# Performance work log

Measured on AMD Instinct MI355X. Metric: run time of the kernel, lower is better.

Reference implementation:

```python
import jax, jax.numpy as jnp
import numpy as np

T, B, C, H, L = 256, 128, 512, 512, 2
WSCALE = 0.03  # keep gates out of hard saturation


def setup_inputs() -> dict:
    key = jax.random.key(0)
    k1, k2, k3 = jax.random.split(key, 3)
    return {
        "input_tensor": jax.random.normal(k1, (T, B, C), jnp.float32),  # (t, b, c), batch_first=False
        "h0": jnp.zeros((L, 4, B, H), jnp.float32),  # per layer: h, c, h_inner, c_inner
        "Wg": jax.random.normal(k2, (L, 4 * H, C + H), jnp.float32) * WSCALE,  # outer Gates
        "bg": jnp.zeros((L, 4 * H), jnp.float32),
        "Wi": jax.random.normal(k3, (L, 4 * H, 2 * H), jnp.float32) * WSCALE,  # inner LSTMCell Gates
        "bi": jnp.zeros((L, 4 * H), jnp.float32),
    }


def _nested_lstm_layer(x, state, Wg, bg, Wi, bi):
    # x: [T, B, C]; state: (h, c, h_inner, c_inner) each [B, H]
    def step(carry, x_t):
        h, c, hi, ci = carry
        # outer cell gates
        g = jnp.concatenate([x_t, h], axis=1) @ Wg.T + bg  # [B, 4H]
        i, f, o, gc = jnp.split(g, 4, axis=1)
        cell = jax.nn.sigmoid(f) * c + jax.nn.sigmoid(i) * jnp.tanh(gc)
        # inner LSTMCell, input = outer candidate cell
        g2 = jnp.concatenate([cell, hi], axis=1) @ Wi.T + bi  # [B, 4H]
        i2, f2, o2, g2c = jnp.split(g2, 4, axis=1)
        ci_n = jax.nn.sigmoid(f2) * ci + jax.nn.sigmoid(i2) * jnp.tanh(g2c)
        hi_n = jax.nn.sigmoid(o2) * jnp.tanh(ci_n)
        # outer cell state is replaced by inner hidden; outer hidden gated on it
        h_n = jax.nn.sigmoid(o) * jnp.tanh(hi_n)
        return (h_n, hi_n, hi_n, ci_n), h_n

    carry, ys = jax.lax.scan(step, state, x)
    return ys, carry  # ys: [T, B, H]


def reference(input_tensor, h0, Wg, bg, Wi, bi):
    x = input_tensor  # already (t, b, c); scan over leading time axis
    n_layers = Wg.shape[0]
    for l in range(n_layers):
        state = (h0[l, 0], h0[l, 1], h0[l, 2], h0[l, 3])
        x, _ = _nested_lstm_layer(x, state, Wg[l], bg[l], Wi[l], bi[l])
    # return_all_layers=False -> last layer output, shape (t, b, h)
    return x
```

## Files before the change

### kernel.cpp

```cpp
#include <hip/hip_runtime.h>

#define T_DIM 256
#define B_DIM 128
#define C_DIM 512
#define H_DIM 512

#define R0H 0
#define R1H 16384
#define R2H 32768
#define PLB 98304

typedef _Float16 half8 __attribute__((ext_vector_type(8)));
typedef float f32x4 __attribute__((ext_vector_type(4)));
typedef unsigned u32x4 __attribute__((ext_vector_type(4)));

__device__ __forceinline__ float sigf(float x) { return 1.0f / (1.0f + __expf(-x)); }
__device__ __forceinline__ float tanhf_(float x) {
  float e = __expf(2.0f * x);
  return (e - 1.0f) / (e + 1.0f);
}

__device__ __forceinline__ half8 cvt8(float4 a, float4 b) {
  half8 h;
  h[0] = (_Float16)a.x; h[1] = (_Float16)a.y; h[2] = (_Float16)a.z; h[3] = (_Float16)a.w;
  h[4] = (_Float16)b.x; h[5] = (_Float16)b.y; h[6] = (_Float16)b.z; h[7] = (_Float16)b.w;
  return h;
}

__device__ __forceinline__ void gbar_arrive(unsigned* slots, int bc, unsigned epoch) {
  __syncthreads();
  if (threadIdx.x == 0) *(volatile unsigned*)(slots + bc) = epoch;
}

__device__ __forceinline__ void gbar_wait_pw(const unsigned* slots, unsigned epoch,
                                             int pollwave) {
  if ((int)(threadIdx.x >> 6) == pollwave) {
    const volatile unsigned* myslot =
        (const volatile unsigned*)(slots + (threadIdx.x & 31));
    int guard = 0;
    for (;;) {
      asm volatile("buffer_inv sc0\n\ts_waitcnt vmcnt(0)" ::: "memory");
      unsigned v = *myslot;
      if (__ballot(v >= epoch) == ~0ull) break;
      if (++guard > (1 << 14)) break;
    }
  }
  __syncthreads();
  asm volatile("buffer_inv sc0" ::: "memory");
  asm volatile("s_waitcnt vmcnt(0)" ::: "memory");
}

__device__ __forceinline__ unsigned sysld_u32(const unsigned* p) {
  unsigned v;
  asm volatile("global_load_dword %0, %1, off sc0 sc1\n\ts_waitcnt vmcnt(0)"
               : "=v"(v) : "v"(p) : "memory");
  return v;
}

__device__ __forceinline__ void xpoll_raw(const unsigned* slots, unsigned epoch) {
  const unsigned* my = slots + (threadIdx.x & 31);
  int guard = 0;
  for (;;) {
    unsigned v = sysld_u32(my);
    if (__ballot(v >= epoch) == ~0ull) break;
    if (++guard > (1 << 15)) break;
  }
}

__device__ __forceinline__ void xpost(unsigned* flag, unsigned epoch) {
  asm volatile("s_waitcnt vmcnt(0)" ::: "memory");
  asm volatile("global_store_dword %0, %1, off sc0 sc1" ::
                   "v"(flag), "v"(epoch) : "memory");
}

__device__ __forceinline__ void store_llc_h16(_Float16* p, _Float16 v) {
  unsigned u = (unsigned)__builtin_bit_cast(unsigned short, v);
  asm volatile("global_store_short %0, %1, off sc0 sc1" ::
                   "v"(p), "v"(u) : "memory");
}

__global__ __launch_bounds__(256, 1) void nlstm_pipe(
    const float* __restrict__ xin, const float* __restrict__ h0,
    const float* __restrict__ Wg, const float* __restrict__ bgb,
    const float* __restrict__ Wi, const float* __restrict__ bib,
    float* __restrict__ out, unsigned* __restrict__ bar,
    _Float16* __restrict__ y0buf, _Float16* __restrict__ hlcb,
    _Float16* __restrict__ hicb, _Float16* __restrict__ clcb)
{
  __shared__ __align__(16) char smem[131072];
  _Float16* AldsH = (_Float16*)smem;
  float* Pl = (float*)(smem + PLB);

  const int tid  = threadIdx.x;
  const int xcd  = blockIdx.x & 7;
  const int lyr  = xcd >> 2;
  const int pgrp = xcd & 3;
  const int bc   = blockIdx.x >> 3;
  const int wv   = tid >> 6;
  const int lane = tid & 63;
  const int ln   = lane & 15;
  const int kg   = lane >> 4;
  const int pb   = tid >> 4;
  const int pj   = tid & 15;
  const int jglob = bc * 16 + pj;
  const int ncol  = bc * 16 + ln;
  const int r0    = pgrp * 32;

  const int exo = (jglob >> 5) * 1024 + (((jglob >> 3) & 3) * 16 + pb) * 8 + (jglob & 7);

  unsigned* eslots = bar + xcd * 64;
  unsigned* cslots = eslots + 32;
  unsigned* fwdS = bar + 512 + pgrp * 32;
  unsigned* bakS = bar + 640 + pgrp * 32;

  _Float16* hloc0 = hlcb + ((size_t)xcd * 2 + 0) * 16384;
  _Float16* hloc1 = hlcb + ((size_t)xcd * 2 + 1) * 16384;
  _Float16* hilc0 = hicb + ((size_t)xcd * 2 + 0) * 16384;
  _Float16* hilc1 = hicb + ((size_t)xcd * 2 + 1) * 16384;
  _Float16* cbase = clcb + (size_t)xcd * 16384;
  _Float16* y0base = y0buf + (size_t)pgrp * 4 * 16384;

  half8 wgf[4][8], wif[4][8];
  float bgv[4], biv[4];
#pragma unroll
  for (int g = 0; g < 4; ++g) {
    const float* wgr = Wg + ((size_t)lyr * 2048 + g * 512 + ncol) * 1024 + wv * 256;
    const float* wir = Wi + ((size_t)lyr * 2048 + g * 512 + ncol) * 1024 + wv * 256;
#pragma unroll
    for (int i = 0; i < 8; ++i) {
      const float* p = wgr + i * 32 + kg * 8;
      wgf[g][i] = cvt8(*(const float4*)p, *(const float4*)(p + 4));
      const float* q = wir + i * 32 + kg * 8;
      wif[g][i] = cvt8(*(const float4*)q, *(const float4*)(q + 4));
    }
    bgv[g] = bgb[lyr * 2048 + g * 512 + jglob];
    biv[g] = bib[lyr * 2048 + g * 512 + jglob];
  }

  float st_c[2], st_ci[2], o_pre[2];
  {
    const float* h0l = h0 + (size_t)lyr * 4 * B_DIM * H_DIM + (size_t)(r0 + pb) * H_DIM + jglob;
#pragma unroll
    for (int mt = 0; mt < 2; ++mt) {
      const float* pp = h0l + (size_t)mt * 16 * H_DIM;
      float h_in  = pp[0];
      st_c[mt]    = pp[(size_t)1 * B_DIM * H_DIM];
      float hi_in = pp[(size_t)2 * B_DIM * H_DIM];
      st_ci[mt]   = pp[(size_t)3 * B_DIM * H_DIM];
      hloc0[exo + mt * 512] = (_Float16)h_in;
      hilc0[exo + mt * 512] = (_Float16)hi_in;
      o_pre[mt] = 0.f;
    }
  }

  auto stage_x = [&](int t) {
    const int m = tid & 31;
    const int q = tid >> 5;
    const int mt = m >> 4, mm = m & 15;
    const float* srow = xin + ((size_t)t * B_DIM + r0 + m) * C_DIM;
#pragma unroll
    for (int i = 0; i < 8; ++i) {
      const int chunk = q * 8 + i;
      const int ks = chunk >> 2, kq = chunk & 3;
      const float* p = srow + chunk * 8;
      *(half8*)(AldsH + R0H + ks * 1024 + mt * 512 + (kq * 16 + mm) * 8) =
          cvt8(*(const float4*)p, *(const float4*)(p + 4));
    }
  };
  auto copy_hhi = [&](const _Float16* hrd, const _Float16* hird) {
    u32x4 vh[8], vy[8];
#pragma unroll
    for (int i = 0; i < 8; ++i) vh[i] = *(const u32x4*)(hrd + (i * 256 + tid) * 8);
#pragma unroll
    for (int i = 0; i < 8; ++i) vy[i] = *(const u32x4*)(hird + (i * 256 + tid) * 8);
#pragma unroll
    for (int i = 0; i < 8; ++i) *(u32x4*)(AldsH + R1H + (i * 256 + tid) * 8) = vh[i];
#pragma unroll
    for (int i = 0; i < 8; ++i) *(u32x4*)(AldsH + R2H + (i * 256 + tid) * 8) = vy[i];
  };
  auto copy_r0 = [&](const _Float16* src) {
    u32x4 v[8];
#pragma unroll
    for (int i = 0; i < 8; ++i) v[i] = *(const u32x4*)(src + (i * 256 + tid) * 8);
#pragma unroll
    for (int i = 0; i < 8; ++i) *(u32x4*)(AldsH + R0H + (i * 256 + tid) * 8) = v[i];
  };
  auto copy_r0_sys = [&](const _Float16* src) {
    u32x4 v[8];
#pragma unroll
    for (int i = 0; i < 8; ++i) {
      const u32x4* p = (const u32x4*)(src + (i * 256 + tid) * 8);
      asm volatile("global_load_dwordx4 %0, %1, off sc0 sc1"
                   : "=v"(v[i]) : "v"(p) : "memory");
    }
    asm volatile("s_waitcnt vmcnt(0)" ::: "memory");
    __builtin_amdgcn_sched_barrier(0);
#pragma unroll
    for (int i = 0; i < 8; ++i)
      *(u32x4*)(AldsH + R0H + (i * 256 + tid) * 8) = v[i];
  };
  auto mfma8 = [&](const _Float16* rb, int ksb, half8 (&wf)[4][8], f32x4 (&acc)[2][4]) {
#pragma unroll
    for (int i = 0; i < 8; ++i) {
      const _Float16* ab = rb + (ksb + i) * 1024 + lane * 8;
      half8 a0 = *(const half8*)(ab);
      half8 a1 = *(const half8*)(ab + 512);
#pragma unroll
      for (int g = 0; g < 4; ++g) {
        acc[0][g] = __builtin_amdgcn_mfma_f32_16x16x32_f16(a0, wf[g][i], acc[0][g], 0, 0, 0);
        acc[1][g] = __builtin_amdgcn_mfma_f32_16x16x32_f16(a1, wf[g][i], acc[1][g], 0, 0, 0);
      }
    }
  };
  auto plw = [&](f32x4 (&acc)[2][4]) {
#pragma unroll
    for (int mt = 0; mt < 2; ++mt)
#pragma unroll
      for (int g = 0; g < 4; ++g)
#pragma unroll
        for (int rr = 0; rr < 4; ++rr)
          Pl[(((g * 2 + mt) * 16 + kg * 4 + rr) * 16 + ln) * 4 + (wv ^ kg)] = acc[mt][g][rr];
  };
  auto plsum = [&](int g, int mt) -> float {
    f32x4 v = *(const f32x4*)(Pl + (((g * 2 + mt) * 16 + pb) * 16 + pj) * 4);
    return v[0] + v[1] + v[2] + v[3];
  };

  unsigned eseq = 0, cseq = 0;

  gbar_arrive(eslots, bc, ++eseq);
  if (lyr == 0) stage_x(0);
  gbar_wait_pw(eslots, eseq, 3);
  if (lyr == 1) {
    if (wv == 0) xpoll_raw(fwdS, 1u);
    __syncthreads();
    copy_r0_sys(y0base + 0);
    __syncthreads();
    if (tid == 0) xpost(bakS + bc, 1u);
  }
  if (wv < 2) {
    f32x4 acc[2][4];
#pragma unroll
    for (int mt = 0; mt < 2; ++mt)
#pragma unroll
      for (int g = 0; g < 4; ++g) acc[mt][g] = (f32x4){0.f, 0.f, 0.f, 0.f};
    mfma8(AldsH + R0H, 8 * wv, wgf, acc);
    plw(acc);
  }

  for (int t = 0; t < T_DIM; ++t) {
    const int pr = t & 1;
    _Float16* hrd  = pr ? hloc1 : hloc0;
    _Float16* hwr  = pr ? hloc0 : hloc1;
    _Float16* hird = pr ? hilc1 : hilc0;
    _Float16* hiwr = pr ? hilc0 : hilc1;
    _Float16* y0wr = y0base + (size_t)(t & 3) * 16384;
    _Float16* y0rd = y0base + (size_t)((t + 1) & 3) * 16384;

    copy_hhi(hrd, hird);
    __syncthreads();

    if (wv >= 2) {
      f32x4 acc[2][4];
#pragma unroll
      for (int mt = 0; mt < 2; ++mt)
#pragma unroll
        for (int g = 0; g < 4; ++g) acc[mt][g] = (f32x4){0.f, 0.f, 0.f, 0.f};
      mfma8(AldsH + R1H, 8 * wv - 16, wgf, acc);
      plw(acc);
    }
    __syncthreads();

#pragma unroll
    for (int mt = 0; mt < 2; ++mt) {
      float gi = plsum(0, mt) + bgv[0];
      float gf = plsum(1, mt) + bgv[1];
      float go = plsum(2, mt) + bgv[2];
      float gc = plsum(3, mt) + bgv[3];
      float cell = sigf(gf) * st_c[mt] + sigf(gi) * tanhf_(gc);
      o_pre[mt] = go;
      cbase[exo + mt * 512] = (_Float16)cell;
    }
    gbar_arrive(cslots, bc, ++cseq);
    if (wv >= 2) {
      f32x4 acc[2][4];
#pragma unroll
      for (int mt = 0; mt < 2; ++mt)
#pragma unroll
        for (int g = 0; g < 4; ++g) acc[mt][g] = (f32x4){0.f, 0.f, 0.f, 0.f};
      mfma8(AldsH + R2H, 8 * wv - 16, wif, acc);
      plw(acc);
    }
    gbar_wait_pw(cslots, cseq, 0);

    copy_r0(cbase);
    __syncthreads();

    if (wv < 2) {
      f32x4 acc[2][4];
#pragma unroll
      for (int mt = 0; mt < 2; ++mt)
#pragma unroll
        for (int g = 0; g < 4; ++g) acc[mt][g] = (f32x4){0.f, 0.f, 0.f, 0.f};
      mfma8(AldsH + R0H, 8 * wv, wif, acc);
      plw(acc);
    }
    __syncthreads();

#pragma unroll
    for (int mt = 0; mt < 2; ++mt) {
      float i2 = plsum(0, mt) + biv[0];
      float f2 = plsum(1, mt) + biv[1];
      float o2 = plsum(2, mt) + biv[2];
      float c2 = plsum(3, mt) + biv[3];
      float ci_n = sigf(f2) * st_ci[mt] + sigf(i2) * tanhf_(c2);
      float hi_n = sigf(o2) * tanhf_(ci_n);
      float h_n  = sigf(o_pre[mt]) * tanhf_(hi_n);
      st_ci[mt] = ci_n;
      st_c[mt]  = hi_n;
      hiwr[exo + mt * 512] = (_Float16)hi_n;
      hwr[exo + mt * 512]  = (_Float16)h_n;
      if (lyr == 0) {
        store_llc_h16(y0wr + exo + mt * 512, (_Float16)h_n);
      } else {
        out[((size_t)t * B_DIM + (r0 + pb + mt * 16)) * H_DIM + jglob] = h_n;
      }
    }

    gbar_arrive(eslots, bc, ++eseq);
    if (lyr == 0) {
      if (tid == 0) xpost(fwdS + bc, (unsigned)(t + 1));
      if (t + 1 < T_DIM) {
        stage_x(t + 1);
        __syncthreads();
        if (wv < 2) {
          f32x4 acc[2][4];
#pragma unroll
          for (int mt = 0; mt < 2; ++mt)
#pragma unroll
            for (int g = 0; g < 4; ++g) acc[mt][g] = (f32x4){0.f, 0.f, 0.f, 0.f};
          mfma8(AldsH + R0H, 8 * wv, wgf, acc);
          plw(acc);
        } else if (wv == 3 && t >= 2) {
          xpoll_raw(bakS, (unsigned)(t - 2));
        }
      }
    } else if (t + 1 < T_DIM) {
      if (wv == 0) xpoll_raw(fwdS, (unsigned)(t + 2));
      __syncthreads();
      copy_r0_sys(y0rd);
      __syncthreads();
      if (tid == 0) xpost(bakS + bc, (unsigned)(t + 2));
      if (wv < 2) {
        f32x4 acc[2][4];
#pragma unroll
        for (int mt = 0; mt < 2; ++mt)
#pragma unroll
          for (int g = 0; g < 4; ++g) acc[mt][g] = (f32x4){0.f, 0.f, 0.f, 0.f};
        mfma8(AldsH + R0H, 8 * wv, wgf, acc);
        plw(acc);
      }
    }
    gbar_wait_pw(eslots, eseq, 3);
  }
}

extern "C" void kernel_launch(void* const* d_in, const int* in_sizes, int n_in,
                              void* d_out, int out_size, void* d_ws, size_t ws_size,
                              hipStream_t stream) {
  const float* xin = (const float*)d_in[0];
  const float* h0  = (const float*)d_in[1];
  const float* Wg  = (const float*)d_in[2];
  const float* bg  = (const float*)d_in[3];
  const float* Wi  = (const float*)d_in[4];
  const float* bi  = (const float*)d_in[5];
  float* out = (float*)d_out;

  unsigned* bar  = (unsigned*)d_ws;
  _Float16* y0b  = (_Float16*)((char*)d_ws + 4096);
  _Float16* hlcb = y0b + (size_t)4 * 4 * 16384;
  _Float16* hicb = hlcb + (size_t)8 * 2 * 16384;
  _Float16* clcb = hicb + (size_t)8 * 2 * 16384;

  hipMemsetAsync(d_ws, 0, 4096, stream);

  nlstm_pipe<<<dim3(256), dim3(256), 0, stream>>>(
      xin, h0, Wg, bg, Wi, bi, out, bar, y0b, hlcb, hicb, clcb);
}
```

Baseline: 2.412 ms.

## Feed MFMA operands directly from global state buffers instead of LDS staging

The per-step copies of h, h_inner and the cell buffer into shared memory are removed, along with their block barriers. The MFMA routine now reads these operands straight from the global ping-pong buffers, and shared memory shrinks to 64KB. Layer-1 output stores are also deferred until after the barrier arrive, so they no longer sit on the critical path. The trade-off is that matrix operands now come from L2 with higher latency inside the inner MFMA loop rather than from LDS.

```diff
diff --git a/kernel.cpp b/kernel.cpp
--- a/kernel.cpp
+++ b/kernel.cpp
@@ -6,9 +6,7 @@
 #define H_DIM 512
 
 #define R0H 0
-#define R1H 16384
-#define R2H 32768
-#define PLB 98304
+#define PLB 32768
 
 typedef _Float16 half8 __attribute__((ext_vector_type(8)));
 typedef float f32x4 __attribute__((ext_vector_type(4)));
@@ -87,7 +85,7 @@
     _Float16* __restrict__ y0buf, _Float16* __restrict__ hlcb,
     _Float16* __restrict__ hicb, _Float16* __restrict__ clcb)
 {
-  __shared__ __align__(16) char smem[131072];
+  __shared__ __align__(16) char smem[65536];
   _Float16* AldsH = (_Float16*)smem;
   float* Pl = (float*)(smem + PLB);
 
@@ -137,7 +135,7 @@
     biv[g] = bib[lyr * 2048 + g * 512 + jglob];
   }
 
-  float st_c[2], st_ci[2], o_pre[2];
+  float st_c[2], st_ci[2], o_pre[2], outv[2];
   {
     const float* h0l = h0 + (size_t)lyr * 4 * B_DIM * H_DIM + (size_t)(r0 + pb) * H_DIM + jglob;
 #pragma unroll
@@ -150,6 +148,7 @@
       hloc0[exo + mt * 512] = (_Float16)h_in;
       hilc0[exo + mt * 512] = (_Float16)hi_in;
       o_pre[mt] = 0.f;
+      outv[mt] = 0.f;
     }
   }
 
@@ -166,24 +165,6 @@
       *(half8*)(AldsH + R0H + ks * 1024 + mt * 512 + (kq * 16 + mm) * 8) =
           cvt8(*(const float4*)p, *(const float4*)(p + 4));
     }
-  };
-  auto copy_hhi = [&](const _Float16* hrd, const _Float16* hird) {
-    u32x4 vh[8], vy[8];
-#pragma unroll
-    for (int i = 0; i < 8; ++i) vh[i] = *(const u32x4*)(hrd + (i * 256 + tid) * 8);
-#pragma unroll
-    for (int i = 0; i < 8; ++i) vy[i] = *(const u32x4*)(hird + (i * 256 + tid) * 8);
-#pragma unroll
-    for (int i = 0; i < 8; ++i) *(u32x4*)(AldsH + R1H + (i * 256 + tid) * 8) = vh[i];
-#pragma unroll
-    for (int i = 0; i < 8; ++i) *(u32x4*)(AldsH + R2H + (i * 256 + tid) * 8) = vy[i];
-  };
-  auto copy_r0 = [&](const _Float16* src) {
-    u32x4 v[8];
-#pragma unroll
-    for (int i = 0; i < 8; ++i) v[i] = *(const u32x4*)(src + (i * 256 + tid) * 8);
-#pragma unroll
-    for (int i = 0; i < 8; ++i) *(u32x4*)(AldsH + R0H + (i * 256 + tid) * 8) = v[i];
   };
   auto copy_r0_sys = [&](const _Float16* src) {
     u32x4 v[8];
@@ -257,16 +238,13 @@
     _Float16* y0wr = y0base + (size_t)(t & 3) * 16384;
     _Float16* y0rd = y0base + (size_t)((t + 1) & 3) * 16384;
 
-    copy_hhi(hrd, hird);
-    __syncthreads();
-
     if (wv >= 2) {
       f32x4 acc[2][4];
 #pragma unroll
       for (int mt = 0; mt < 2; ++mt)
 #pragma unroll
         for (int g = 0; g < 4; ++g) acc[mt][g] = (f32x4){0.f, 0.f, 0.f, 0.f};
-      mfma8(AldsH + R1H, 8 * wv - 16, wgf, acc);
+      mfma8(hrd, 8 * wv - 16, wgf, acc);
       plw(acc);
     }
     __syncthreads();
@@ -288,13 +266,10 @@
       for (int mt = 0; mt < 2; ++mt)
 #pragma unroll
         for (int g = 0; g < 4; ++g) acc[mt][g] = (f32x4){0.f, 0.f, 0.f, 0.f};
-      mfma8(AldsH + R2H, 8 * wv - 16, wif, acc);
+      mfma8(hird, 8 * wv - 16, wif, acc);
       plw(acc);
     }
     gbar_wait_pw(cslots, cseq, 0);
-
-    copy_r0(cbase);
-    __syncthreads();
 
     if (wv < 2) {
       f32x4 acc[2][4];
@@ -302,7 +277,7 @@
       for (int mt = 0; mt < 2; ++mt)
 #pragma unroll
         for (int g = 0; g < 4; ++g) acc[mt][g] = (f32x4){0.f, 0.f, 0.f, 0.f};
-      mfma8(AldsH + R0H, 8 * wv, wif, acc);
+      mfma8(cbase, 8 * wv, wif, acc);
       plw(acc);
     }
     __syncthreads();
@@ -323,7 +298,7 @@
       if (lyr == 0) {
         store_llc_h16(y0wr + exo + mt * 512, (_Float16)h_n);
       } else {
-        out[((size_t)t * B_DIM + (r0 + pb + mt * 16)) * H_DIM + jglob] = h_n;
+        outv[mt] = h_n;
       }
     }
 
@@ -345,20 +320,25 @@
           xpoll_raw(bakS, (unsigned)(t - 2));
         }
       }
-    } else if (t + 1 < T_DIM) {
-      if (wv == 0) xpoll_raw(fwdS, (unsigned)(t + 2));
-      __syncthreads();
-      copy_r0_sys(y0rd);
-      __syncthreads();
-      if (tid == 0) xpost(bakS + bc, (unsigned)(t + 2));
-      if (wv < 2) {
-        f32x4 acc[2][4];
-#pragma unroll
-        for (int mt = 0; mt < 2; ++mt)
-#pragma unroll
-          for (int g = 0; g < 4; ++g) acc[mt][g] = (f32x4){0.f, 0.f, 0.f, 0.f};
-        mfma8(AldsH + R0H, 8 * wv, wgf, acc);
-        plw(acc);
+    } else {
+#pragma unroll
+      for (int mt = 0; mt < 2; ++mt)
+        out[((size_t)t * B_DIM + (r0 + pb + mt * 16)) * H_DIM + jglob] = outv[mt];
+      if (t + 1 < T_DIM) {
+        if (wv == 0) xpoll_raw(fwdS, (unsigned)(t + 2));
+        __syncthreads();
+        copy_r0_sys(y0rd);
+        __syncthreads();
+        if (tid == 0) xpost(bakS + bc, (unsigned)(t + 2));
+        if (wv < 2) {
+          f32x4 acc[2][4];
+#pragma unroll
+          for (int mt = 0; mt < 2; ++mt)
+#pragma unroll
+            for (int g = 0; g < 4; ++g) acc[mt][g] = (f32x4){0.f, 0.f, 0.f, 0.f};
+          mfma8(AldsH + R0H, 8 * wv, wgf, acc);
+          plw(acc);
+        }
       }
     }
     gbar_wait_pw(eslots, eseq, 3);
```

Measured after the change: 2.592 ms. 1.07x slower.
